# Optimization experiments

Hardware: AMD Instinct MI355X
Metric: run time of the kernel (lower is better)

The kernel has to match this reference:

```python
import jax, jax.numpy as jnp
import numpy as np

D_K = 64
SCALE = jnp.sqrt(jnp.float32(D_K))

def setup_inputs() -> dict:
    key = jax.random.key(0)
    kq, kk, kv = jax.random.split(key, 3)
    shape = (2, 16, 2048, D_K)  # [batch, heads, seq, d_k]
    return {
        "Q": jax.random.normal(kq, shape, dtype=jnp.float32),
        "K": jax.random.normal(kk, shape, dtype=jnp.float32),
        "V": jax.random.normal(kv, shape, dtype=jnp.float32),
    }

def reference(Q, K, V):
    # scores: [B, H, S, S]
    scores = jnp.einsum("bhqd,bhkd->bhqk", Q, K) / SCALE
    weights = jax.nn.softmax(scores, axis=-1)
    return jnp.einsum("bhqk,bhkd->bhqd", weights, V)
```

## Files before the change

### kernel.cpp

```cpp
#include <hip/hip_runtime.h>
#include <math.h>

#define S_LEN 2048
#define DK 64
#define BH 32
#define BQ 128
#define BK 64
#define NT 32
#define NTH 16
#define TILE_US 8192
#define TILE_B  16384

#if defined(__has_builtin)
#if __has_builtin(__builtin_amdgcn_exp2f)
#define EXP2F(x) __builtin_amdgcn_exp2f(x)
#else
#define EXP2F(x) exp2f(x)
#endif
#else
#define EXP2F(x) exp2f(x)
#endif

typedef _Float16 f16x8 __attribute__((ext_vector_type(8)));
typedef __fp16   fp16x2 __attribute__((ext_vector_type(2)));
typedef float    f32x16 __attribute__((ext_vector_type(16)));

#define MFMAH(a,b,c) __builtin_amdgcn_mfma_f32_32x32x16_f16((a),(b),(c),0,0,0)

union U16H { uint4 u; f16x8 h; unsigned short s[8]; };

__device__ __forceinline__ f16x8 ldsh8(const unsigned short* p){
    U16H t; t.u = *(const uint4*)p; return t.h;
}
__device__ __forceinline__ f16x8 u4h(unsigned a, unsigned b, unsigned c, unsigned d){
    U16H t; t.u = make_uint4(a,b,c,d); return t.h;
}
__device__ __forceinline__ unsigned pk16(float a, float b){
    union { fp16x2 h; unsigned u; } c;
    c.h = __builtin_amdgcn_cvt_pkrtz(a, b);
    return c.u;
}
__device__ __forceinline__ unsigned short f16b(float x){
    union { _Float16 f; unsigned short s; } c; c.f = (_Float16)x; return c.s;
}
__device__ __forceinline__ void gl_lds16(const void* g, void* l){
    __builtin_amdgcn_global_load_lds(
        (const __attribute__((address_space(1))) void*)g,
        (__attribute__((address_space(3))) void*)l, 16, 0, 0);
}

__global__ __launch_bounds__(256) void prep(const float* __restrict__ K,
                                            const float* __restrict__ V,
                                            unsigned short* __restrict__ W) {
    __shared__ unsigned short Vt[64 * 72];
    const int t = threadIdx.x;
    const int head = blockIdx.x >> 5;
    const int kb = blockIdx.x & 31;
    const size_t hbase = (size_t)head * S_LEN * DK;
    unsigned short* Wt = W + (size_t)(head * NT + kb) * TILE_US;

    {
        const int row = t >> 2;
        const int c0 = (t & 3) * 16;
        const float* vp = V + hbase + (size_t)(kb * BK + row) * DK + c0;
        #pragma unroll
        for (int i = 0; i < 4; ++i) {
            const float4 q = *(const float4*)(vp + 4 * i);
            const int c = c0 + 4 * i;
            Vt[(c + 0) * 72 + row] = f16b(q.x);
            Vt[(c + 1) * 72 + row] = f16b(q.y);
            Vt[(c + 2) * 72 + row] = f16b(q.z);
            Vt[(c + 3) * 72 + row] = f16b(q.w);
        }
    }
    #pragma unroll
    for (int i = 0; i < 2; ++i) {
        const int P = i * 256 + t;
        const int r = P >> 3, p = P & 7;
        const int ch = p ^ (r & 7);
        const float* kp = K + hbase + (size_t)(kb * BK + r) * DK + ch * 8;
        const float4 a = *(const float4*)kp;
        const float4 b = *(const float4*)(kp + 4);
        *(uint4*)(Wt + P * 8) = make_uint4(pk16(a.x, a.y), pk16(a.z, a.w),
                                           pk16(b.x, b.y), pk16(b.z, b.w));
    }
    __syncthreads();
    #pragma unroll
    for (int i = 0; i < 2; ++i) {
        const int P = i * 256 + t;
        const int d = P >> 3, p = P & 7;
        const int ch = p ^ (d & 7);
        const uint4 u = *(const uint4*)(Vt + d * 72 + ch * 8);
        *(uint4*)(Wt + 4096 + P * 8) = u;
    }
}

__global__ __launch_bounds__(256, 2) void fa4(const float* __restrict__ Q,
                                              const unsigned short* __restrict__ W,
                                              float* __restrict__ O) {
    __shared__ __align__(16) unsigned short SB[4 * TILE_US];
    __shared__ float Lbuf[BQ];

    const int tid = threadIdx.x;
    const int kh  = tid >> 7;
    const int wq  = (tid >> 6) & 1;
    const int lane = tid & 63;
    const int L31 = tid & 31;
    const int q5  = (tid >> 5) & 1;
    const int swz = L31 & 7;

    const int bid  = blockIdx.x;
    const int x    = bid & 7, g = bid >> 3;
    const int head = ((g >> 4) << 3) | x;
    const int qb   = g & 15;
    const size_t hbase = (size_t)head * S_LEN * DK;
    const unsigned short* Wh = W + (size_t)head * NT * TILE_US;
    unsigned short* SBh = SB + kh * 2 * TILE_US;

    const float c1 = 0.18033688011112042f;
    f16x8 qfA[4], qfB[4];
    {
        const int qrow = qb * BQ + wq * 64 + L31;
        const float* qpA = Q + hbase + (size_t)qrow * DK;
        const float* qpB = qpA + 32 * DK;
        #pragma unroll
        for (int ks = 0; ks < 4; ++ks) {
            float4 a = *(const float4*)(qpA + ks * 16 + q5 * 8);
            float4 b = *(const float4*)(qpA + ks * 16 + q5 * 8 + 4);
            qfA[ks] = u4h(pk16(a.x * c1, a.y * c1), pk16(a.z * c1, a.w * c1),
                          pk16(b.x * c1, b.y * c1), pk16(b.z * c1, b.w * c1));
            a = *(const float4*)(qpB + ks * 16 + q5 * 8);
            b = *(const float4*)(qpB + ks * 16 + q5 * 8 + 4);
            qfB[ks] = u4h(pk16(a.x * c1, a.y * c1), pk16(a.z * c1, a.w * c1),
                          pk16(b.x * c1, b.y * c1), pk16(b.z * c1, b.w * c1));
        }
    }

    {
        const char* src = (const char*)Wh + (size_t)(kh * NTH) * TILE_B + wq * 8192 + lane * 16;
        char* dst = (char*)SBh + wq * 8192;
        #pragma unroll
        for (int j = 0; j < 8; ++j) gl_lds16(src + j * 1024, dst + j * 1024);
    }
    __syncthreads();

    f32x16 oA0 = {}, oA1 = {}, oB0 = {}, oB1 = {};
    float lA = 0.f, lB = 0.f;

    for (int it = 0; it < NTH; ++it) {
        const int cur = it & 1;
        if (it + 1 < NTH) {
            const char* src = (const char*)Wh + (size_t)(kh * NTH + it + 1) * TILE_B + wq * 8192 + lane * 16;
            char* dst = (char*)SBh + (cur ^ 1) * TILE_B + wq * 8192;
            #pragma unroll
            for (int j = 0; j < 8; ++j) gl_lds16(src + j * 1024, dst + j * 1024);
        }
        const unsigned short* B0 = SBh + cur * TILE_US;

        f32x16 sA0 = {}, sA1 = {}, sB0 = {}, sB1 = {};
        #pragma unroll
        for (int ks = 0; ks < 4; ++ks) {
            const int ch = ((ks * 2 + q5) ^ swz) * 8;
            const unsigned short* pk_ = B0 + L31 * 64 + ch;
            const f16x8 a0 = ldsh8(pk_);
            const f16x8 a1 = ldsh8(pk_ + 2048);
            sA0 = MFMAH(a0, qfA[ks], sA0);
            sA1 = MFMAH(a1, qfA[ks], sA1);
            sB0 = MFMAH(a0, qfB[ks], sB0);
            sB1 = MFMAH(a1, qfB[ks], sB1);
        }

        float ra0 = 0.f, ra1 = 0.f, rb0 = 0.f, rb1 = 0.f;
        #pragma unroll
        for (int r = 0; r < 16; ++r) {
            sA0[r] = EXP2F(sA0[r]); ra0 += sA0[r];
            sA1[r] = EXP2F(sA1[r]); ra1 += sA1[r];
            sB0[r] = EXP2F(sB0[r]); rb0 += sB0[r];
            sB1[r] = EXP2F(sB1[r]); rb1 += sB1[r];
        }
        float rsA = ra0 + ra1;
        float rsB = rb0 + rb1;
        rsA += __shfl_xor(rsA, 32); lA += rsA;
        rsB += __shfl_xor(rsB, 32); lB += rsB;

        unsigned PA[2][4][2], PB[2][4][2];
        #pragma unroll
        for (int b = 0; b < 4; ++b) {
            PA[0][b][0] = pk16(sA0[4*b+0], sA0[4*b+1]);
            PA[0][b][1] = pk16(sA0[4*b+2], sA0[4*b+3]);
            PA[1][b][0] = pk16(sA1[4*b+0], sA1[4*b+1]);
            PA[1][b][1] = pk16(sA1[4*b+2], sA1[4*b+3]);
            PB[0][b][0] = pk16(sB0[4*b+0], sB0[4*b+1]);
            PB[0][b][1] = pk16(sB0[4*b+2], sB0[4*b+3]);
            PB[1][b][0] = pk16(sB1[4*b+0], sB1[4*b+1]);
            PB[1][b][1] = pk16(sB1[4*b+2], sB1[4*b+3]);
        }

        #pragma unroll
        for (int ks = 0; ks < 4; ++ks) {
            const int mt = ks >> 1, kk2 = (ks & 1) * 2;
            const int ch = ((ks * 2 + q5) ^ swz) * 8;
            const unsigned short* pv = B0 + 4096 + L31 * 64 + ch;
            const f16x8 v0 = ldsh8(pv);
            const f16x8 v1 = ldsh8(pv + 2048);
            {
                const unsigned own0 = q5 ? PA[mt][kk2+1][0] : PA[mt][kk2][0];
                const unsigned own1 = q5 ? PA[mt][kk2+1][1] : PA[mt][kk2][1];
                const unsigned snd0 = q5 ? PA[mt][kk2][0]   : PA[mt][kk2+1][0];
                const unsigned snd1 = q5 ? PA[mt][kk2][1]   : PA[mt][kk2+1][1];
                const unsigned r0 = (unsigned)__shfl_xor((int)snd0, 32);
                const unsigned r1 = (unsigned)__shfl_xor((int)snd1, 32);
                const f16x8 ph = q5 ? u4h(r0, r1, own0, own1) : u4h(own0, own1, r0, r1);
                oA0 = MFMAH(v0, ph, oA0);
                oA1 = MFMAH(v1, ph, oA1);
            }
            {
                const unsigned own0 = q5 ? PB[mt][kk2+1][0] : PB[mt][kk2][0];
                const unsigned own1 = q5 ? PB[mt][kk2+1][1] : PB[mt][kk2][1];
                const unsigned snd0 = q5 ? PB[mt][kk2][0]   : PB[mt][kk2+1][0];
                const unsigned snd1 = q5 ? PB[mt][kk2][1]   : PB[mt][kk2+1][1];
                const unsigned r0 = (unsigned)__shfl_xor((int)snd0, 32);
                const unsigned r1 = (unsigned)__shfl_xor((int)snd1, 32);
                const f16x8 ph = q5 ? u4h(r0, r1, own0, own1) : u4h(own0, own1, r0, r1);
                oB0 = MFMAH(v0, ph, oB0);
                oB1 = MFMAH(v1, ph, oB1);
            }
        }
        __syncthreads();
    }

    float* Mbuf = (float*)SB;
    const int qA = wq * 64 + L31;
    if (kh == 1) {
        float* mpA = Mbuf + qA * 68;
        float* mpB = mpA + 32 * 68;
        #pragma unroll
        for (int b = 0; b < 4; ++b) {
            *(float4*)(mpA + 8 * b + 4 * q5) =
                make_float4(oA0[4*b+0], oA0[4*b+1], oA0[4*b+2], oA0[4*b+3]);
            *(float4*)(mpA + 32 + 8 * b + 4 * q5) =
                make_float4(oA1[4*b+0], oA1[4*b+1], oA1[4*b+2], oA1[4*b+3]);
            *(float4*)(mpB + 8 * b + 4 * q5) =
                make_float4(oB0[4*b+0], oB0[4*b+1], oB0[4*b+2], oB0[4*b+3]);
            *(float4*)(mpB + 32 + 8 * b + 4 * q5) =
                make_float4(oB1[4*b+0], oB1[4*b+1], oB1[4*b+2], oB1[4*b+3]);
        }
        if (q5 == 0) { Lbuf[qA] = lA; Lbuf[qA + 32] = lB; }
    }
    __syncthreads();
    if (kh == 0) {
        const float invA = 1.f / (lA + Lbuf[qA]);
        const float invB = 1.f / (lB + Lbuf[qA + 32]);
        const float* mpA = Mbuf + qA * 68;
        const float* mpB = mpA + 32 * 68;
        const int qrow = qb * BQ + qA;
        float* opA = O + hbase + (size_t)qrow * DK;
        float* opB = opA + 32 * DK;
        #pragma unroll
        for (int b = 0; b < 4; ++b) {
            float4 m = *(const float4*)(mpA + 8 * b + 4 * q5);
            float4 o;
            o.x = (oA0[4*b+0] + m.x) * invA; o.y = (oA0[4*b+1] + m.y) * invA;
            o.z = (oA0[4*b+2] + m.z) * invA; o.w = (oA0[4*b+3] + m.w) * invA;
            *(float4*)(opA + 8 * b + 4 * q5) = o;
            m = *(const float4*)(mpA + 32 + 8 * b + 4 * q5);
            o.x = (oA1[4*b+0] + m.x) * invA; o.y = (oA1[4*b+1] + m.y) * invA;
            o.z = (oA1[4*b+2] + m.z) * invA; o.w = (oA1[4*b+3] + m.w) * invA;
            *(float4*)(opA + 32 + 8 * b + 4 * q5) = o;
            m = *(const float4*)(mpB + 8 * b + 4 * q5);
            o.x = (oB0[4*b+0] + m.x) * invB; o.y = (oB0[4*b+1] + m.y) * invB;
            o.z = (oB0[4*b+2] + m.z) * invB; o.w = (oB0[4*b+3] + m.w) * invB;
            *(float4*)(opB + 8 * b + 4 * q5) = o;
            m = *(const float4*)(mpB + 32 + 8 * b + 4 * q5);
            o.x = (oB1[4*b+0] + m.x) * invB; o.y = (oB1[4*b+1] + m.y) * invB;
            o.z = (oB1[4*b+2] + m.z) * invB; o.w = (oB1[4*b+3] + m.w) * invB;
            *(float4*)(opB + 32 + 8 * b + 4 * q5) = o;
        }
    }
}

extern "C" void kernel_launch(void* const* d_in, const int* in_sizes, int n_in,
                              void* d_out, int out_size, void* d_ws, size_t ws_size,
                              hipStream_t stream) {
    const float* Q = (const float*)d_in[0];
    const float* K = (const float*)d_in[1];
    const float* V = (const float*)d_in[2];
    float* O = (float*)d_out;
    unsigned short* W = (unsigned short*)d_ws;
    prep<<<dim3(BH * NT), dim3(256), 0, stream>>>(K, V, W);
    fa4<<<dim3(512), dim3(256), 0, stream>>>(Q, W, O);
}
```

Measured before the change: 137.5 us.

## Load K/V MFMA fragments directly from global into registers, dropping LDS staging

The prep kernel now writes K and V tiles in a per-lane MFMA fragment order, so each lane can fetch its operands with contiguous 16-byte global loads. The attention kernel drops the LDS double buffer, its global_load_lds staging and the per-iteration __syncthreads, and instead prefetches the next tile's K/V fragments into registers. The aim is to remove LDS traffic and block-wide barriers. In exchange it raises register pressure and depends on the L2 cache to absorb the repeated K/V reads from both waves sharing a tile. It also prefetches one tile past the end on the last iteration, an unused read that stays within the allocation except for the final head.

```diff
diff --git a/kernel.cpp b/kernel.cpp
--- a/kernel.cpp
+++ b/kernel.cpp
@@ -29,7 +29,7 @@
 
 union U16H { uint4 u; f16x8 h; unsigned short s[8]; };
 
-__device__ __forceinline__ f16x8 ldsh8(const unsigned short* p){
+__device__ __forceinline__ f16x8 g16(const unsigned short* p){
     U16H t; t.u = *(const uint4*)p; return t.h;
 }
 __device__ __forceinline__ f16x8 u4h(unsigned a, unsigned b, unsigned c, unsigned d){
@@ -42,11 +42,6 @@
 }
 __device__ __forceinline__ unsigned short f16b(float x){
     union { _Float16 f; unsigned short s; } c; c.f = (_Float16)x; return c.s;
-}
-__device__ __forceinline__ void gl_lds16(const void* g, void* l){
-    __builtin_amdgcn_global_load_lds(
-        (const __attribute__((address_space(1))) void*)g,
-        (__attribute__((address_space(3))) void*)l, 16, 0, 0);
 }
 
 __global__ __launch_bounds__(256) void prep(const float* __restrict__ K,
@@ -77,28 +72,30 @@
     for (int i = 0; i < 2; ++i) {
         const int P = i * 256 + t;
         const int r = P >> 3, p = P & 7;
-        const int ch = p ^ (r & 7);
-        const float* kp = K + hbase + (size_t)(kb * BK + r) * DK + ch * 8;
+        const float* kp = K + hbase + (size_t)(kb * BK + r) * DK + p * 8;
         const float4 a = *(const float4*)kp;
         const float4 b = *(const float4*)(kp + 4);
-        *(uint4*)(Wt + P * 8) = make_uint4(pk16(a.x, a.y), pk16(a.z, a.w),
-                                           pk16(b.x, b.y), pk16(b.z, b.w));
+        const int frag  = ((r >> 5) << 2) | (p >> 1);
+        const int lane8 = ((p & 1) << 5) | (r & 31);
+        *(uint4*)(Wt + frag * 512 + lane8 * 8) =
+            make_uint4(pk16(a.x, a.y), pk16(a.z, a.w), pk16(b.x, b.y), pk16(b.z, b.w));
     }
     __syncthreads();
     #pragma unroll
     for (int i = 0; i < 2; ++i) {
         const int P = i * 256 + t;
         const int d = P >> 3, p = P & 7;
-        const int ch = p ^ (d & 7);
-        const uint4 u = *(const uint4*)(Vt + d * 72 + ch * 8);
-        *(uint4*)(Wt + 4096 + P * 8) = u;
+        const uint4 u = *(const uint4*)(Vt + d * 72 + p * 8);
+        const int frag  = 8 + (((d >> 5) << 2) | (p >> 1));
+        const int lane8 = ((p & 1) << 5) | (d & 31);
+        *(uint4*)(Wt + frag * 512 + lane8 * 8) = u;
     }
 }
 
 __global__ __launch_bounds__(256, 2) void fa4(const float* __restrict__ Q,
                                               const unsigned short* __restrict__ W,
                                               float* __restrict__ O) {
-    __shared__ __align__(16) unsigned short SB[4 * TILE_US];
+    __shared__ __align__(16) float Mbuf[BQ * 68];
     __shared__ float Lbuf[BQ];
 
     const int tid = threadIdx.x;
@@ -107,7 +104,6 @@
     const int lane = tid & 63;
     const int L31 = tid & 31;
     const int q5  = (tid >> 5) & 1;
-    const int swz = L31 & 7;
 
     const int bid  = blockIdx.x;
     const int x    = bid & 7, g = bid >> 3;
@@ -115,7 +111,6 @@
     const int qb   = g & 15;
     const size_t hbase = (size_t)head * S_LEN * DK;
     const unsigned short* Wh = W + (size_t)head * NT * TILE_US;
-    unsigned short* SBh = SB + kh * 2 * TILE_US;
 
     const float c1 = 0.18033688011112042f;
     f16x8 qfA[4], qfB[4];
@@ -136,38 +131,37 @@
         }
     }
 
-    {
-        const char* src = (const char*)Wh + (size_t)(kh * NTH) * TILE_B + wq * 8192 + lane * 16;
-        char* dst = (char*)SBh + wq * 8192;
-        #pragma unroll
-        for (int j = 0; j < 8; ++j) gl_lds16(src + j * 1024, dst + j * 1024);
-    }
-    __syncthreads();
+    const unsigned short* tb = Wh + (size_t)(kh * NTH) * TILE_US;
+    const int lo = lane * 8;
+    f16x8 ka[4], kb_[4], va[4], vb[4];
+    #pragma unroll
+    for (int ks = 0; ks < 4; ++ks) {
+        ka[ks]  = g16(tb + ks * 512 + lo);
+        kb_[ks] = g16(tb + (4 + ks) * 512 + lo);
+    }
+    #pragma unroll
+    for (int ks = 0; ks < 4; ++ks) {
+        va[ks] = g16(tb + (8 + ks) * 512 + lo);
+        vb[ks] = g16(tb + (12 + ks) * 512 + lo);
+    }
 
     f32x16 oA0 = {}, oA1 = {}, oB0 = {}, oB1 = {};
     float lA = 0.f, lB = 0.f;
 
     for (int it = 0; it < NTH; ++it) {
-        const int cur = it & 1;
-        if (it + 1 < NTH) {
-            const char* src = (const char*)Wh + (size_t)(kh * NTH + it + 1) * TILE_B + wq * 8192 + lane * 16;
-            char* dst = (char*)SBh + (cur ^ 1) * TILE_B + wq * 8192;
-            #pragma unroll
-            for (int j = 0; j < 8; ++j) gl_lds16(src + j * 1024, dst + j * 1024);
-        }
-        const unsigned short* B0 = SBh + cur * TILE_US;
-
         f32x16 sA0 = {}, sA1 = {}, sB0 = {}, sB1 = {};
         #pragma unroll
         for (int ks = 0; ks < 4; ++ks) {
-            const int ch = ((ks * 2 + q5) ^ swz) * 8;
-            const unsigned short* pk_ = B0 + L31 * 64 + ch;
-            const f16x8 a0 = ldsh8(pk_);
-            const f16x8 a1 = ldsh8(pk_ + 2048);
-            sA0 = MFMAH(a0, qfA[ks], sA0);
-            sA1 = MFMAH(a1, qfA[ks], sA1);
-            sB0 = MFMAH(a0, qfB[ks], sB0);
-            sB1 = MFMAH(a1, qfB[ks], sB1);
+            sA0 = MFMAH(ka[ks],  qfA[ks], sA0);
+            sA1 = MFMAH(kb_[ks], qfA[ks], sA1);
+            sB0 = MFMAH(ka[ks],  qfB[ks], sB0);
+            sB1 = MFMAH(kb_[ks], qfB[ks], sB1);
+        }
+        const unsigned short* nx = tb + TILE_US;
+        #pragma unroll
+        for (int ks = 0; ks < 4; ++ks) {
+            ka[ks]  = g16(nx + ks * 512 + lo);
+            kb_[ks] = g16(nx + (4 + ks) * 512 + lo);
         }
 
         float ra0 = 0.f, ra1 = 0.f, rb0 = 0.f, rb1 = 0.f;
@@ -199,10 +193,8 @@
         #pragma unroll
         for (int ks = 0; ks < 4; ++ks) {
             const int mt = ks >> 1, kk2 = (ks & 1) * 2;
-            const int ch = ((ks * 2 + q5) ^ swz) * 8;
-            const unsigned short* pv = B0 + 4096 + L31 * 64 + ch;
-            const f16x8 v0 = ldsh8(pv);
-            const f16x8 v1 = ldsh8(pv + 2048);
+            const f16x8 v0 = va[ks];
+            const f16x8 v1 = vb[ks];
             {
                 const unsigned own0 = q5 ? PA[mt][kk2+1][0] : PA[mt][kk2][0];
                 const unsigned own1 = q5 ? PA[mt][kk2+1][1] : PA[mt][kk2][1];
@@ -226,10 +218,14 @@
                 oB1 = MFMAH(v1, ph, oB1);
             }
         }
-        __syncthreads();
-    }
-
-    float* Mbuf = (float*)SB;
+        #pragma unroll
+        for (int ks = 0; ks < 4; ++ks) {
+            va[ks] = g16(nx + (8 + ks) * 512 + lo);
+            vb[ks] = g16(nx + (12 + ks) * 512 + lo);
+        }
+        tb = nx;
+    }
+
     const int qA = wq * 64 + L31;
     if (kh == 1) {
         float* mpA = Mbuf + qA * 68;
```

Result: slower. 140.9 us (+2.5%).
